# Kernel optimization log

Hardware: AMD Instinct MI355X
Metric: run time of the kernel (lower is better)

The kernel has to match this reference:

```python
import jax, jax.numpy as jnp
import numpy as np

B, S, D, H = 2, 2048, 1024, 16
DK = D // H


def setup_inputs() -> dict:
    key = jax.random.key(0)
    ks = jax.random.split(key, 12)
    std = 1.0 / np.sqrt(D)
    inp = {
        "query": jax.random.normal(ks[0], (B, S, D), jnp.float32),
        "key": jax.random.normal(ks[1], (B, S, D), jnp.float32),
        "value": jax.random.normal(ks[2], (B, S, D), jnp.float32),
        # causal decoder mask [B, 1, S, S]; 0 -> masked
        "mask": jnp.broadcast_to(jnp.tril(jnp.ones((S, S), jnp.int32)), (B, 1, S, S)),
        "wq": jax.random.uniform(ks[3], (D, D), jnp.float32, -std, std),
        "bq": jax.random.uniform(ks[4], (D,), jnp.float32, -std, std),
        "wk": jax.random.uniform(ks[5], (D, D), jnp.float32, -std, std),
        "bk": jax.random.uniform(ks[6], (D,), jnp.float32, -std, std),
        "wv": jax.random.uniform(ks[7], (D, D), jnp.float32, -std, std),
        "bv": jax.random.uniform(ks[8], (D,), jnp.float32, -std, std),
        "wo": jax.random.uniform(ks[9], (D, D), jnp.float32, -std, std),
        "bo": jax.random.uniform(ks[10], (D,), jnp.float32, -std, std),
    }
    return inp


def _split_heads(x):
    b, s, _ = x.shape
    return x.reshape(b, s, H, DK).transpose(0, 2, 1, 3)  # [B,H,S,DK]


def reference(query, key, value, mask, wq, bq, wk, bk, wv, bv, wo, bo):
    # nn.Linear: y = x @ W^T + b
    q = _split_heads(query @ wq.T + bq)
    k = _split_heads(key @ wk.T + bk)
    v = _split_heads(value @ wv.T + bv)
    scores = jnp.einsum("bhqd,bhkd->bhqk", q, k) / np.sqrt(DK).astype(np.float32)
    scores = jnp.where(mask == 0, jnp.float32(-1e9), scores)
    attn = jax.nn.softmax(scores, axis=-1)
    # dropout is identity in eval mode
    out = jnp.einsum("bhqk,bhkd->bhqd", attn, v)
    out = out.transpose(0, 2, 1, 3).reshape(query.shape[0], -1, D)
    return out @ wo.T + bo
```

## Files before the change

### kernel.cpp

```cpp
#include <hip/hip_runtime.h>
#include <hip/hip_bf16.h>
#include <cstdint>
#include <cstddef>

#define B_ 2
#define S_ 2048
#define D_ 1024
#define H_ 16
#define DK_ 64

#define AS1 __attribute__((address_space(1)))
#define AS3 __attribute__((address_space(3)))

typedef __attribute__((ext_vector_type(8))) short short8;
typedef __attribute__((ext_vector_type(4))) float f32x4;
typedef __attribute__((ext_vector_type(16))) float f32x16;
typedef __attribute__((ext_vector_type(4))) unsigned short ushort4_t;

__device__ __forceinline__ unsigned short f2bf(float f) {
    union { float f; unsigned u; } x; x.f = f;
    unsigned r = x.u + 0x7fffu + ((x.u >> 16) & 1u);
    return (unsigned short)(r >> 16);
}

__device__ __forceinline__ unsigned pack_bf16(float lo, float hi_) {
    union { __hip_bfloat162 h; unsigned u; } cv;
    cv.h = __float22bfloat162_rn(make_float2(lo, hi_));
    return cv.u;
}

__device__ __forceinline__ float xor32f(float x, int hi) {
#if __has_builtin(__builtin_amdgcn_permlane32_swap)
    unsigned u = __builtin_bit_cast(unsigned, x);
    auto r = __builtin_amdgcn_permlane32_swap(u, u, false, false);
    return __builtin_bit_cast(float, hi ? r[0] : r[1]);
#else
    return __shfl_xor(x, 32);
#endif
}

__device__ __forceinline__ void swap32(unsigned a, unsigned b, unsigned& x, unsigned& y, int hi) {
#if __has_builtin(__builtin_amdgcn_permlane32_swap)
    auto r = __builtin_amdgcn_permlane32_swap(a, b, false, false);
    x = r[0]; y = r[1];
#else
    unsigned pa_ = __shfl_xor(a, 32), pb_ = __shfl_xor(b, 32);
    x = hi ? pb_ : a;
    y = hi ? b : pa_;
#endif
}

__global__ __launch_bounds__(256) void cvt_act(
    const float* __restrict__ q, const float* __restrict__ k, const float* __restrict__ v,
    unsigned short* __restrict__ xq, unsigned short* __restrict__ xk,
    unsigned short* __restrict__ xv) {
    int b = blockIdx.x;
    int which = b >> 11, rel = b & 2047;
    const float* src = (which == 0) ? q : (which == 1) ? k : v;
    unsigned short* dst = (which == 0) ? xq : (which == 1) ? xk : xv;
    int i = rel * 256 + threadIdx.x;
    const float4* s4 = (const float4*)src;
    float4 a = s4[2 * i], c = s4[2 * i + 1];
    short8 o;
    o[0] = (short)f2bf(a.x); o[1] = (short)f2bf(a.y); o[2] = (short)f2bf(a.z); o[3] = (short)f2bf(a.w);
    o[4] = (short)f2bf(c.x); o[5] = (short)f2bf(c.y); o[6] = (short)f2bf(c.z); o[7] = (short)f2bf(c.w);
    *(short8*)(dst + (size_t)i * 8) = o;
}

template <int OUTMODE>
__device__ __forceinline__ void gemm_body(const unsigned short* __restrict__ Ab,
                                          const float* __restrict__ Wf,
                                          const float* __restrict__ bias,
                                          void* __restrict__ Cout, float scale,
                                          unsigned short* __restrict__ As0,
                                          unsigned short* __restrict__ As1,
                                          unsigned short* __restrict__ Bs) {
    constexpr int Kd = 1024;
    const int t = threadIdx.x;
    const int l = t & 63;
    const int l15 = l & 15, l4 = l >> 4;
    const int wid = t >> 6;
    const int wm = wid >> 1, wn = wid & 1;
    const int m0 = (blockIdx.x * 4 + (blockIdx.y & 3)) * 128;
    const int n0 = (blockIdx.y >> 2) * 128;

    f32x4 acc[4][4] = {};

    int ldsoff[4];
    int sgo[4];
#pragma unroll
    for (int p = 0; p < 4; p++) {
        int off = p * 4096 + t * 16;
        int row = off >> 7;
        int slot = (off >> 4) & 7;
        ldsoff[p] = off;
        sgo[p] = row * Kd + (slot ^ (row & 7)) * 8;
    }

#define GLOADA(BUF, K0)                                                               \
    { _Pragma("unroll") for (int p = 0; p < 4; p++)                                   \
        __builtin_amdgcn_global_load_lds(                                             \
            (const AS1 void*)(Ab + (size_t)m0 * Kd + sgo[p] + (K0)),                  \
            (AS3 void*)((char*)(BUF) + ldsoff[p]), 16, 0, 0); }
#define LOADW(DST, K0)                                                                \
    { _Pragma("unroll") for (int p = 0; p < 4; p++) {                                 \
        const float* s_ = Wf + (size_t)n0 * Kd + sgo[p] + (K0);                       \
        DST[p][0] = *(const float4*)(s_);                                             \
        DST[p][1] = *(const float4*)(s_ + 4); } }
#define CVTSTW(SRC)                                                                   \
    { _Pragma("unroll") for (int p = 0; p < 4; p++) {                                 \
        short8 o_;                                                                    \
        o_[0] = (short)f2bf(SRC[p][0].x); o_[1] = (short)f2bf(SRC[p][0].y);           \
        o_[2] = (short)f2bf(SRC[p][0].z); o_[3] = (short)f2bf(SRC[p][0].w);           \
        o_[4] = (short)f2bf(SRC[p][1].x); o_[5] = (short)f2bf(SRC[p][1].y);           \
        o_[6] = (short)f2bf(SRC[p][1].z); o_[7] = (short)f2bf(SRC[p][1].w);           \
        *(short8*)((char*)Bs + ldsoff[p]) = o_; } }

#define GEMMSTEP(CURBUF, NXTBUF, CW, NW, K0)                                          \
    {                                                                                 \
        if ((K0) + 64 < Kd) { GLOADA(NXTBUF, (K0) + 64); LOADW(NW, (K0) + 64); }      \
        __builtin_amdgcn_sched_barrier(0);  \
        CVTSTW(CW);                                                                   \
        asm volatile("s_waitcnt lgkmcnt(0)" ::: "memory");                            \
        if ((K0) + 64 >= Kd) { asm volatile("s_waitcnt vmcnt(0)" ::: "memory"); }     \
        __builtin_amdgcn_sched_barrier(0);                                            \
        __builtin_amdgcn_s_barrier();                                                 \
        __builtin_amdgcn_sched_barrier(0);                                            \
        _Pragma("unroll") for (int kk = 0; kk < 2; kk++) {                            \
            short8 af[4], bfr[4];                                                     \
            _Pragma("unroll") for (int mi = 0; mi < 4; mi++) {                        \
                int row = wm * 64 + mi * 16 + l15;                                    \
                int slot = kk * 4 + l4;                                               \
                af[mi] = *(const short8*)((const char*)(CURBUF) + row * 128 +         \
                                          ((slot ^ (row & 7)) << 4));                 \
            }                                                                         \
            _Pragma("unroll") for (int ni = 0; ni < 4; ni++) {                        \
                int row = wn * 64 + ni * 16 + l15;                                    \
                int slot = kk * 4 + l4;                                               \
                bfr[ni] = *(const short8*)((const char*)Bs + row * 128 +              \
                                           ((slot ^ (row & 7)) << 4));                \
            }                                                                         \
            _Pragma("unroll") for (int mi = 0; mi < 4; mi++)                          \
                _Pragma("unroll") for (int ni = 0; ni < 4; ni++)                      \
                    acc[mi][ni] = __builtin_amdgcn_mfma_f32_16x16x32_bf16(            \
                        af[mi], bfr[ni], acc[mi][ni], 0, 0, 0);                       \
        }                                                                             \
        __builtin_amdgcn_s_barrier();                                                 \
        __builtin_amdgcn_sched_barrier(0);                                            \
    }

    float4 wvA[4][2], wvB[4][2];
    GLOADA(As0, 0);
    LOADW(wvA, 0);

    for (int k0 = 0; k0 < Kd; k0 += 128) {
        GEMMSTEP(As0, As1, wvA, wvB, k0);
        GEMMSTEP(As1, As0, wvB, wvA, k0 + 64);
    }
#undef GEMMSTEP
#undef CVTSTW
#undef LOADW
#undef GLOADA

#pragma unroll
    for (int mi = 0; mi < 4; mi++) {
#pragma unroll
        for (int ni = 0; ni < 4; ni++) {
            int n = n0 + wn * 64 + ni * 16 + l15;
            float bn = bias[n];
            int mb = m0 + wm * 64 + mi * 16 + l4 * 4;
            if constexpr (OUTMODE == 2) {
                int b = mb >> 11, s = mb & 2047, h = n >> 6, dk = n & 63;
                ushort4_t vv;
#pragma unroll
                for (int j = 0; j < 4; j++) vv[j] = f2bf(acc[mi][ni][j] + bn);
                *(ushort4_t*)((unsigned short*)Cout + ((size_t)(b * H_ + h) * DK_ + dk) * S_ + s) = vv;
            } else {
#pragma unroll
                for (int j = 0; j < 4; j++) {
                    float v = (acc[mi][ni][j] + bn) * scale;
                    int m = mb + j;
                    if constexpr (OUTMODE == 0) {
                        int b = m >> 11, s = m & 2047, h = n >> 6, dk = n & 63;
                        ((unsigned short*)Cout)[(((size_t)b * H_ + h) * S_ + s) * DK_ + dk] = f2bf(v);
                    } else {
                        ((float*)Cout)[(size_t)m * D_ + n] = v;
                    }
                }
            }
        }
    }
}

__global__ __launch_bounds__(256, 2) void qkv_gemm(
    const unsigned short* __restrict__ xq, const unsigned short* __restrict__ xk,
    const unsigned short* __restrict__ xv,
    const float* __restrict__ wq, const float* __restrict__ wk, const float* __restrict__ wv,
    const float* __restrict__ bq, const float* __restrict__ bk, const float* __restrict__ bv,
    unsigned short* __restrict__ qo, unsigned short* __restrict__ ko, unsigned short* __restrict__ vto,
    float qscale) {
    __shared__ unsigned short As[2][128 * 64];
    __shared__ unsigned short Bs[128 * 64];
    int z = blockIdx.z;
    if (z == 2) {
        gemm_body<2>(xv, wv, bv, vto, 1.0f, As[0], As[1], Bs);
    } else if (z == 0) {
        gemm_body<0>(xq, wq, bq, qo, qscale, As[0], As[1], Bs);
    } else {
        gemm_body<0>(xk, wk, bk, ko, 1.0f, As[0], As[1], Bs);
    }
}

__global__ __launch_bounds__(256, 2) void out_gemm(const unsigned short* __restrict__ Aa,
                                                   const float* __restrict__ Wo,
                                                   const float* __restrict__ bo,
                                                   float* __restrict__ out) {
    __shared__ unsigned short As[2][128 * 64];
    __shared__ unsigned short Bs[128 * 64];
    gemm_body<1>(Aa, Wo, bo, out, 1.0f, As[0], As[1], Bs);
}

union AttnSm {
    unsigned short kv[2][2][128 * 64];
    struct { float obuf[2][2][32][64]; float lArr[2][4][32]; } m;
};

__device__ __forceinline__ void attn_compute(const short8 kf[4], const short8 vf[4],
                                             const short8 qf[4], int lq, int hi, bool diag,
                                             f32x16& o0, f32x16& o1, float& l_run) {
    f32x16 sT = {};
    __builtin_amdgcn_s_setprio(1);
#pragma unroll
    for (int c = 0; c < 4; c++)
        sT = __builtin_amdgcn_mfma_f32_32x32x16_bf16(kf[c], qf[c], sT, 0, 0, 0);
    __builtin_amdgcn_s_setprio(0);

    float e[16];
#pragma unroll
    for (int r = 0; r < 16; r++) e[r] = exp2f(sT[r]);
    if (diag) {
#pragma unroll
        for (int r = 0; r < 16; r++) {
            int kvl = (r & 3) + 8 * (r >> 2) + 4 * hi;
            e[r] = (kvl <= lq) ? e[r] : 0.0f;
        }
    }

    float s8[8];
#pragma unroll
    for (int r = 0; r < 8; r++) s8[r] = e[2 * r] + e[2 * r + 1];
#pragma unroll
    for (int r = 0; r < 4; r++) s8[r] = s8[r] + s8[r + 4];
    float ps = (s8[0] + s8[1]) + (s8[2] + s8[3]);
    ps += xor32f(ps, hi);
    l_run += ps;

    unsigned OW[8];
#pragma unroll
    for (int w = 0; w < 8; w++) OW[w] = pack_bf16(e[2 * w], e[2 * w + 1]);

    union { unsigned u[4]; short8 s; } pa0, pa1;
    swap32(OW[0], OW[2], pa0.u[0], pa0.u[2], hi);
    swap32(OW[1], OW[3], pa0.u[1], pa0.u[3], hi);
    swap32(OW[4], OW[6], pa1.u[0], pa1.u[2], hi);
    swap32(OW[5], OW[7], pa1.u[1], pa1.u[3], hi);

    __builtin_amdgcn_s_setprio(1);
    o0 = __builtin_amdgcn_mfma_f32_32x32x16_bf16(pa0.s, vf[0], o0, 0, 0, 0);
    o1 = __builtin_amdgcn_mfma_f32_32x32x16_bf16(pa0.s, vf[1], o1, 0, 0, 0);
    o0 = __builtin_amdgcn_mfma_f32_32x32x16_bf16(pa1.s, vf[2], o0, 0, 0, 0);
    o1 = __builtin_amdgcn_mfma_f32_32x32x16_bf16(pa1.s, vf[3], o1, 0, 0, 0);
    __builtin_amdgcn_s_setprio(0);
}

__global__ __launch_bounds__(512, 4) void attn_kernel(const unsigned short* __restrict__ Q,
                                                      const unsigned short* __restrict__ Kk,
                                                      const unsigned short* __restrict__ Vt,
                                                      unsigned short* __restrict__ Aout) {
    __shared__ AttnSm sm;

    const int t_ = threadIdx.x;
    const int l = t_ & 63;
    const int w = t_ >> 6;
    const int qsub = w >> 2, kvw = w & 3;
    const int lq = l & 31, hi = l >> 5;

    const int bid = blockIdx.x;
    const int xcd = bid & 7, j = bid >> 3;
    const int bh = xcd * 4 + (j >> 5);
    const int bq = 31 - (j & 31);
    const int wq0 = bq * 64;
    const int qi = 2 * bq + qsub;
    const int T = ((2 * bq + 1) >> 2) + 1;

    const unsigned short* Qh = Q + (size_t)bh * S_ * DK_;
    const unsigned short* Kh = Kk + (size_t)bh * S_ * DK_;
    const unsigned short* Vth = Vt + (size_t)bh * DK_ * S_;

    short8 qf[4];
    const unsigned short* qrow = Qh + (size_t)(wq0 + qsub * 32 + lq) * DK_ + hi * 8;
#pragma unroll
    for (int c = 0; c < 4; c++) qf[c] = *(const short8*)(qrow + 16 * c);

    f32x16 o0 = {}, o1 = {};
    float l_run = 0.f;

    const int lr = kvw * 32 + lq;
    unsigned kaddr[4], vaddr[4];
#pragma unroll
    for (int c = 0; c < 4; c++)
        kaddr[c] = (unsigned)(lr * 128 + (((2 * c + hi) ^ (lr & 7)) << 4));
#pragma unroll
    for (int c = 0; c < 2; c++) {
        unsigned sl = (unsigned)(((kvw * 4 + 2 * c + hi) ^ (lq & 15)) << 4);
        vaddr[2 * c] = (unsigned)(lq * 256) + sl;
        vaddr[2 * c + 1] = (unsigned)((lq + 32) * 256) + sl;
    }

    const int off0 = t_ * 16, off1 = 8192 + t_ * 16;
    int ldsoff[2] = {off0, off1};
    const char* kgp[2];
    const char* vgp[2];
#pragma unroll
    for (int p = 0; p < 2; p++) {
        int off = (p == 0) ? off0 : off1;
        int rk = off >> 7, slk = (off >> 4) & 7;
        kgp[p] = (const char*)Kh + rk * 128 + ((slk ^ (rk & 7)) << 4);
        int rv = off >> 8, slv = (off >> 4) & 15;
        vgp[p] = (const char*)Vth + (size_t)rv * (S_ * 2) + ((slv ^ (rv & 15)) << 4);
    }

#define STAGE(BUF)                                                                      \
    {                                                                                   \
        _Pragma("unroll") for (int p = 0; p < 2; p++) {                                 \
            __builtin_amdgcn_global_load_lds((const AS1 void*)kgp[p],                   \
                (AS3 void*)((char*)sm.kv[BUF][0] + ldsoff[p]), 16, 0, 0);               \
            kgp[p] += 128 * DK_ * 2;                          \
        }                                                                               \
        _Pragma("unroll") for (int p = 0; p < 2; p++) {                                 \
            __builtin_amdgcn_global_load_lds((const AS1 void*)vgp[p],                   \
                (AS3 void*)((char*)sm.kv[BUF][1] + ldsoff[p]), 16, 0, 0);               \
            vgp[p] += 128 * 2;                     \
        }                                                                               \
    }

#define TILE_STEP(BUF, T_IDX)                                                           \
    {                                                                                   \
        if ((T_IDX) + 1 < T) { asm volatile("s_waitcnt vmcnt(4)" ::: "memory"); }       \
        else                 { asm volatile("s_waitcnt vmcnt(0)" ::: "memory"); }       \
        __builtin_amdgcn_sched_barrier(0);                                              \
        __builtin_amdgcn_s_barrier();                                                   \
        __builtin_amdgcn_sched_barrier(0);                                              \
        const int sidx = 4 * (T_IDX) + kvw;                                             \
        if (sidx <= qi) {                                                               \
            short8 kf[4], vf[4];                                                        \
            const char* Kbuf = (const char*)sm.kv[BUF][0];                              \
            const char* Vbuf = (const char*)sm.kv[BUF][1];                              \
            _Pragma("unroll") for (int c = 0; c < 4; c++)                               \
                kf[c] = *(const short8*)(Kbuf + kaddr[c]);                              \
            _Pragma("unroll") for (int c = 0; c < 4; c++)                               \
                vf[c] = *(const short8*)(Vbuf + vaddr[c]);                              \
            attn_compute(kf, vf, qf, lq, hi, sidx == qi, o0, o1, l_run);                \
        }                                                                               \
        asm volatile("s_waitcnt lgkmcnt(0)" ::: "memory");                              \
        __builtin_amdgcn_sched_barrier(0);                                              \
        __builtin_amdgcn_s_barrier();                                                   \
        __builtin_amdgcn_sched_barrier(0);                                              \
        if ((T_IDX) + 2 < T) STAGE(BUF);                                                \
    }

    STAGE(0);
    STAGE(1);

    for (int t = 0; t < T; t += 2) {
        TILE_STEP(0, t);
        if (t + 1 < T) TILE_STEP(1, t + 1);
    }
#undef TILE_STEP
#undef STAGE

    float(&obuf)[2][2][32][64] = sm.m.obuf;
    float(&lArr)[2][4][32] = sm.m.lArr;
    if (hi == 0) lArr[qsub][kvw][lq] = l_run;

    if (kvw < 2) {
#pragma unroll
        for (int r = 0; r < 16; r++) {
            int qrw = (r & 3) + 8 * (r >> 2) + 4 * hi;
            obuf[qsub][kvw][qrw][lq] = o0[r];
            obuf[qsub][kvw][qrw][lq + 32] = o1[r];
        }
    }
    __syncthreads();
    if (kvw >= 2) {
#pragma unroll
        for (int r = 0; r < 16; r++) {
            int qrw = (r & 3) + 8 * (r >> 2) + 4 * hi;
            obuf[qsub][kvw - 2][qrw][lq] += o0[r];
            obuf[qsub][kvw - 2][qrw][lq + 32] += o1[r];
        }
    }
    __syncthreads();

    const int b = bh >> 4, h = bh & 15;
    const int row = (w & 3) * 8 + (l >> 3);
    const int dk0 = (l & 7) * 8;
    float ls = lArr[qsub][0][row] + lArr[qsub][1][row] + lArr[qsub][2][row] + lArr[qsub][3][row];
    float inv = 1.0f / ls;
    short8 ov;
#pragma unroll
    for (int jj = 0; jj < 8; jj++) {
        float s = obuf[qsub][0][row][dk0 + jj] + obuf[qsub][1][row][dk0 + jj];
        ov[jj] = (short)f2bf(s * inv);
    }
    unsigned short* orow = Aout + ((size_t)b * S_ + (wq0 + qsub * 32 + row)) * D_ + h * 64 + dk0;
    *(short8*)orow = ov;
}

extern "C" void kernel_launch(void* const* d_in, const int* in_sizes, int n_in,
                              void* d_out, int out_size, void* d_ws, size_t ws_size,
                              hipStream_t stream) {
    const float* query = (const float*)d_in[0];
    const float* key = (const float*)d_in[1];
    const float* value = (const float*)d_in[2];
    const float* wq = (const float*)d_in[4];
    const float* bq = (const float*)d_in[5];
    const float* wk = (const float*)d_in[6];
    const float* bk = (const float*)d_in[7];
    const float* wv = (const float*)d_in[8];
    const float* bv = (const float*)d_in[9];
    const float* wo = (const float*)d_in[10];
    const float* bo = (const float*)d_in[11];

    const size_t NX = (size_t)B_ * S_ * D_;
    char* p = (char*)d_ws;
    unsigned short* xq = (unsigned short*)p; p += NX * 2;
    unsigned short* xk = (unsigned short*)p; p += NX * 2;
    unsigned short* xv = (unsigned short*)p; p += NX * 2;
    unsigned short* qb = (unsigned short*)p; p += NX * 2;
    unsigned short* kb = (unsigned short*)p; p += NX * 2;
    unsigned short* vtb = (unsigned short*)p; p += NX * 2;
    unsigned short* ab = (unsigned short*)p; p += NX * 2;

    cvt_act<<<dim3(6144), dim3(256), 0, stream>>>(query, key, value, xq, xk, xv);

    const float qscale = 0.125f * 1.4426950408889634f;
    qkv_gemm<<<dim3(8, 32, 3), dim3(256), 0, stream>>>(xq, xk, xv, wq, wk, wv,
                                                       bq, bk, bv, qb, kb, vtb, qscale);
    attn_kernel<<<dim3(1024), dim3(512), 0, stream>>>(qb, kb, vtb, ab);
    out_gemm<<<dim3(8, 32), dim3(256), 0, stream>>>(ab, wo, bo, (float*)d_out);
}
```

Measured before the change: 127.4 us.

## Pre-convert weights to bf16 and stream both GEMM operands via async LDS loads

The four weight matrices are now converted to bf16 in the same up-front conversion kernel as the activations. The GEMM loop no longer loads fp32 weights into registers and converts them before storing to LDS. Both A and B tiles are fetched with global_load_lds into double-buffered LDS, and a partial vmcnt wait lets the next tile's loads overlap the current MFMAs. This removes per-tile conversion work and register pressure in the GEMMs, halves weight read traffic, and deepens the pipeline. The cost is an extra weight conversion pass, more workspace, and double the B tile LDS footprint.

```diff
diff --git a/kernel.cpp b/kernel.cpp
--- a/kernel.cpp
+++ b/kernel.cpp
@@ -50,14 +50,24 @@
 #endif
 }
 
-__global__ __launch_bounds__(256) void cvt_act(
+__global__ __launch_bounds__(256) void cvt_all(
     const float* __restrict__ q, const float* __restrict__ k, const float* __restrict__ v,
-    unsigned short* __restrict__ xq, unsigned short* __restrict__ xk,
-    unsigned short* __restrict__ xv) {
+    const float* __restrict__ wq, const float* __restrict__ wk, const float* __restrict__ wv,
+    const float* __restrict__ wo,
+    unsigned short* __restrict__ xq, unsigned short* __restrict__ xk, unsigned short* __restrict__ xv,
+    unsigned short* __restrict__ wqb, unsigned short* __restrict__ wkb, unsigned short* __restrict__ wvb,
+    unsigned short* __restrict__ wob) {
     int b = blockIdx.x;
-    int which = b >> 11, rel = b & 2047;
-    const float* src = (which == 0) ? q : (which == 1) ? k : v;
-    unsigned short* dst = (which == 0) ? xq : (which == 1) ? xk : xv;
+    const float* src; unsigned short* dst; int rel;
+    if (b < 6144) {
+        int which = b >> 11; rel = b & 2047;
+        src = (which == 0) ? q : (which == 1) ? k : v;
+        dst = (which == 0) ? xq : (which == 1) ? xk : xv;
+    } else {
+        int bb = b - 6144; int which = bb >> 9; rel = bb & 511;
+        src = (which == 0) ? wq : (which == 1) ? wk : (which == 2) ? wv : wo;
+        dst = (which == 0) ? wqb : (which == 1) ? wkb : (which == 2) ? wvb : wob;
+    }
     int i = rel * 256 + threadIdx.x;
     const float4* s4 = (const float4*)src;
     float4 a = s4[2 * i], c = s4[2 * i + 1];
@@ -69,12 +79,13 @@
 
 template <int OUTMODE>
 __device__ __forceinline__ void gemm_body(const unsigned short* __restrict__ Ab,
-                                          const float* __restrict__ Wf,
+                                          const unsigned short* __restrict__ Wb,
                                           const float* __restrict__ bias,
                                           void* __restrict__ Cout, float scale,
                                           unsigned short* __restrict__ As0,
                                           unsigned short* __restrict__ As1,
-                                          unsigned short* __restrict__ Bs) {
+                                          unsigned short* __restrict__ Bs0,
+                                          unsigned short* __restrict__ Bs1) {
     constexpr int Kd = 1024;
     const int t = threadIdx.x;
     const int l = t & 63;
@@ -97,32 +108,26 @@
         sgo[p] = row * Kd + (slot ^ (row & 7)) * 8;
     }
 
-#define GLOADA(BUF, K0)                                                               \
-    { _Pragma("unroll") for (int p = 0; p < 4; p++)                                   \
-        __builtin_amdgcn_global_load_lds(                                             \
-            (const AS1 void*)(Ab + (size_t)m0 * Kd + sgo[p] + (K0)),                  \
-            (AS3 void*)((char*)(BUF) + ldsoff[p]), 16, 0, 0); }
-#define LOADW(DST, K0)                                                                \
-    { _Pragma("unroll") for (int p = 0; p < 4; p++) {                                 \
-        const float* s_ = Wf + (size_t)n0 * Kd + sgo[p] + (K0);                       \
-        DST[p][0] = *(const float4*)(s_);                                             \
-        DST[p][1] = *(const float4*)(s_ + 4); } }
-#define CVTSTW(SRC)                                                                   \
-    { _Pragma("unroll") for (int p = 0; p < 4; p++) {                                 \
-        short8 o_;                                                                    \
-        o_[0] = (short)f2bf(SRC[p][0].x); o_[1] = (short)f2bf(SRC[p][0].y);           \
-        o_[2] = (short)f2bf(SRC[p][0].z); o_[3] = (short)f2bf(SRC[p][0].w);           \
-        o_[4] = (short)f2bf(SRC[p][1].x); o_[5] = (short)f2bf(SRC[p][1].y);           \
-        o_[6] = (short)f2bf(SRC[p][1].z); o_[7] = (short)f2bf(SRC[p][1].w);           \
-        *(short8*)((char*)Bs + ldsoff[p]) = o_; } }
-
-#define GEMMSTEP(CURBUF, NXTBUF, CW, NW, K0)                                          \
+#define GLOAD(BUFA, BUFB, K0)                                                         \
     {                                                                                 \
-        if ((K0) + 64 < Kd) { GLOADA(NXTBUF, (K0) + 64); LOADW(NW, (K0) + 64); }      \
-        __builtin_amdgcn_sched_barrier(0);  \
-        CVTSTW(CW);                                                                   \
-        asm volatile("s_waitcnt lgkmcnt(0)" ::: "memory");                            \
-        if ((K0) + 64 >= Kd) { asm volatile("s_waitcnt vmcnt(0)" ::: "memory"); }     \
+        _Pragma("unroll") for (int p = 0; p < 4; p++)                                 \
+            __builtin_amdgcn_global_load_lds(                                         \
+                (const AS1 void*)(Ab + (size_t)m0 * Kd + sgo[p] + (K0)),              \
+                (AS3 void*)((char*)(BUFA) + ldsoff[p]), 16, 0, 0);                    \
+        _Pragma("unroll") for (int p = 0; p < 4; p++)                                 \
+            __builtin_amdgcn_global_load_lds(                                         \
+                (const AS1 void*)(Wb + (size_t)n0 * Kd + sgo[p] + (K0)),              \
+                (AS3 void*)((char*)(BUFB) + ldsoff[p]), 16, 0, 0);                    \
+    }
+
+#define GEMMSTEP(CA, CB, NA, NB, K0)                                                  \
+    {                                                                                 \
+        if ((K0) + 64 < Kd) {                                                         \
+            GLOAD(NA, NB, (K0) + 64);                                                 \
+            asm volatile("s_waitcnt vmcnt(8)" ::: "memory");                          \
+        } else {                                                                      \
+            asm volatile("s_waitcnt vmcnt(0)" ::: "memory");                          \
+        }                                                                             \
         __builtin_amdgcn_sched_barrier(0);                                            \
         __builtin_amdgcn_s_barrier();                                                 \
         __builtin_amdgcn_sched_barrier(0);                                            \
@@ -131,13 +136,13 @@
             _Pragma("unroll") for (int mi = 0; mi < 4; mi++) {                        \
                 int row = wm * 64 + mi * 16 + l15;                                    \
                 int slot = kk * 4 + l4;                                               \
-                af[mi] = *(const short8*)((const char*)(CURBUF) + row * 128 +         \
+                af[mi] = *(const short8*)((const char*)(CA) + row * 128 +             \
                                           ((slot ^ (row & 7)) << 4));                 \
             }                                                                         \
             _Pragma("unroll") for (int ni = 0; ni < 4; ni++) {                        \
                 int row = wn * 64 + ni * 16 + l15;                                    \
                 int slot = kk * 4 + l4;                                               \
-                bfr[ni] = *(const short8*)((const char*)Bs + row * 128 +              \
+                bfr[ni] = *(const short8*)((const char*)(CB) + row * 128 +            \
                                            ((slot ^ (row & 7)) << 4));                \
             }                                                                         \
             _Pragma("unroll") for (int mi = 0; mi < 4; mi++)                          \
@@ -149,18 +154,13 @@
         __builtin_amdgcn_sched_barrier(0);                                            \
     }
 
-    float4 wvA[4][2], wvB[4][2];
-    GLOADA(As0, 0);
-    LOADW(wvA, 0);
-
+    GLOAD(As0, Bs0, 0);
     for (int k0 = 0; k0 < Kd; k0 += 128) {
-        GEMMSTEP(As0, As1, wvA, wvB, k0);
-        GEMMSTEP(As1, As0, wvB, wvA, k0 + 64);
+        GEMMSTEP(As0, Bs0, As1, Bs1, k0);
+        GEMMSTEP(As1, Bs1, As0, Bs0, k0 + 64);
     }
 #undef GEMMSTEP
-#undef CVTSTW
-#undef LOADW
-#undef GLOADA
+#undef GLOAD
 
 #pragma unroll
     for (int mi = 0; mi < 4; mi++) {
@@ -194,30 +194,30 @@
 
 __global__ __launch_bounds__(256, 2) void qkv_gemm(
     const unsigned short* __restrict__ xq, const unsigned short* __restrict__ xk,
-    const unsigned short* __restrict__ xv,
-    const float* __restrict__ wq, const float* __restrict__ wk, const float* __restrict__ wv,
+    const unsigned short* __restrict__ xv, const unsigned short* __restrict__ wqb,
+    const unsigned short* __restrict__ wkb, const unsigned short* __restrict__ wvb,
     const float* __restrict__ bq, const float* __restrict__ bk, const float* __restrict__ bv,
     unsigned short* __restrict__ qo, unsigned short* __restrict__ ko, unsigned short* __restrict__ vto,
     float qscale) {
     __shared__ unsigned short As[2][128 * 64];
-    __shared__ unsigned short Bs[128 * 64];
+    __shared__ unsigned short Bs[2][128 * 64];
     int z = blockIdx.z;
     if (z == 2) {
-        gemm_body<2>(xv, wv, bv, vto, 1.0f, As[0], As[1], Bs);
+        gemm_body<2>(xv, wvb, bv, vto, 1.0f, As[0], As[1], Bs[0], Bs[1]);
     } else if (z == 0) {
-        gemm_body<0>(xq, wq, bq, qo, qscale, As[0], As[1], Bs);
+        gemm_body<0>(xq, wqb, bq, qo, qscale, As[0], As[1], Bs[0], Bs[1]);
     } else {
-        gemm_body<0>(xk, wk, bk, ko, 1.0f, As[0], As[1], Bs);
+        gemm_body<0>(xk, wkb, bk, ko, 1.0f, As[0], As[1], Bs[0], Bs[1]);
     }
 }
 
 __global__ __launch_bounds__(256, 2) void out_gemm(const unsigned short* __restrict__ Aa,
-                                                   const float* __restrict__ Wo,
+                                                   const unsigned short* __restrict__ Wo,
                                                    const float* __restrict__ bo,
                                                    float* __restrict__ out) {
     __shared__ unsigned short As[2][128 * 64];
-    __shared__ unsigned short Bs[128 * 64];
-    gemm_body<1>(Aa, Wo, bo, out, 1.0f, As[0], As[1], Bs);
+    __shared__ unsigned short Bs[2][128 * 64];
+    gemm_body<1>(Aa, Wo, bo, out, 1.0f, As[0], As[1], Bs[0], Bs[1]);
 }
 
 union AttnSm {
@@ -433,20 +433,26 @@
     const float* bo = (const float*)d_in[11];
 
     const size_t NX = (size_t)B_ * S_ * D_;
+    const size_t NW = (size_t)D_ * D_;
     char* p = (char*)d_ws;
     unsigned short* xq = (unsigned short*)p; p += NX * 2;
     unsigned short* xk = (unsigned short*)p; p += NX * 2;
     unsigned short* xv = (unsigned short*)p; p += NX * 2;
+    unsigned short* wqb = (unsigned short*)p; p += NW * 2;
+    unsigned short* wkb = (unsigned short*)p; p += NW * 2;
+    unsigned short* wvb = (unsigned short*)p; p += NW * 2;
+    unsigned short* wob = (unsigned short*)p; p += NW * 2;
     unsigned short* qb = (unsigned short*)p; p += NX * 2;
     unsigned short* kb = (unsigned short*)p; p += NX * 2;
     unsigned short* vtb = (unsigned short*)p; p += NX * 2;
     unsigned short* ab = (unsigned short*)p; p += NX * 2;
 
-    cvt_act<<<dim3(6144), dim3(256), 0, stream>>>(query, key, value, xq, xk, xv);
+    cvt_all<<<dim3(8192), dim3(256), 0, stream>>>(query, key, value, wq, wk, wv, wo,
+                                                  xq, xk, xv, wqb, wkb, wvb, wob);
 
     const float qscale = 0.125f * 1.4426950408889634f;
-    qkv_gemm<<<dim3(8, 32, 3), dim3(256), 0, stream>>>(xq, xk, xv, wq, wk, wv,
+    qkv_gemm<<<dim3(8, 32, 3), dim3(256), 0, stream>>>(xq, xk, xv, wqb, wkb, wvb,
                                                        bq, bk, bv, qb, kb, vtb, qscale);
     attn_kernel<<<dim3(1024), dim3(512), 0, stream>>>(qb, kb, vtb, ab);
-    out_gemm<<<dim3(8, 32), dim3(256), 0, stream>>>(ab, wo, bo, (float*)d_out);
-}
+    out_gemm<<<dim3(8, 32), dim3(256), 0, stream>>>(ab, wob, bo, (float*)d_out);
+}
```

Result: faster. 119.7 us (median of 3 runs) (-6.0%).
